# Optimization experiments

Hardware: AMD Instinct MI355X
Metric: run time of the kernel (lower is better)

The kernel has to match this reference:

```python
import jax, jax.numpy as jnp
import numpy as np

N = 50000       # nodes
E = 800000      # edges (avg degree 16)
R = 8           # relations
IN = 128        # in_channels
H = 128         # hidden_size
B = 10          # graphs in batch
NPG = N // B    # nodes per graph (equal-size graphs)
NEG_SLOPE = 0.2 # RGATConv default negative_slope


def setup_inputs() -> dict:
    key = jax.random.key(0)
    ks = jax.random.split(key, 12)
    s = 0.1
    x = jax.random.normal(ks[0], (N, IN), dtype=jnp.float32)
    edge_index = jax.random.randint(ks[1], (2, E), 0, N, dtype=jnp.int32)
    edge_type = jax.random.randint(ks[2], (E,), 0, R, dtype=jnp.int32)
    batch = jnp.repeat(jnp.arange(B, dtype=jnp.int32), NPG)
    W1 = jax.random.normal(ks[3], (R, IN, H), dtype=jnp.float32) * s
    q1 = jax.random.normal(ks[4], (H, 1), dtype=jnp.float32) * s
    k1 = jax.random.normal(ks[5], (H, 1), dtype=jnp.float32) * s
    b1 = jnp.zeros((H,), dtype=jnp.float32)
    W2 = jax.random.normal(ks[6], (R, H, H), dtype=jnp.float32) * s
    q2 = jax.random.normal(ks[7], (H, 1), dtype=jnp.float32) * s
    k2 = jax.random.normal(ks[8], (H, 1), dtype=jnp.float32) * s
    b2 = jnp.zeros((H,), dtype=jnp.float32)
    Wl = jax.random.normal(ks[9], (H, H), dtype=jnp.float32) * s
    bl = jnp.zeros((H,), dtype=jnp.float32)
    return dict(x=x, edge_index=edge_index, edge_type=edge_type, batch=batch,
                W1=W1, q1=q1, k1=k1, b1=b1, W2=W2, q2=q2, k2=k2, b2=b2,
                Wl=Wl, bl=bl)


def _rgat_conv(x, src, tgt, etype, W, q, k, b):
    # Per-relation transform once per node ([R,N,H]), then gather per edge;
    # mathematically identical to PyG's per-edge bmm but avoids the [E,in,H] blowup.
    xW = jnp.einsum('ni,rio->rno', x, W)          # [R, N, H]
    outi = xW[etype, tgt]                          # [E, H] transformed target feats
    outj = xW[etype, src]                          # [E, H] transformed source feats
    # additive self-attention, heads=1, dim=1
    alpha = jax.nn.leaky_relu(outi @ q + outj @ k, NEG_SLOPE)  # [E, 1]
    # across-relation segment softmax over incoming edges of each target node
    m = jax.ops.segment_max(alpha, tgt, num_segments=N)        # [N, 1]
    a = jnp.exp(alpha - m[tgt])
    den = jax.ops.segment_sum(a, tgt, num_segments=N)          # [N, 1]
    a = a / (den[tgt] + 1e-16)
    out = jax.ops.segment_sum(a * outj, tgt, num_segments=N)   # [N, H]
    return out + b


def reference(x, edge_index, edge_type, batch, W1, q1, k1, b1,
              W2, q2, k2, b2, Wl, bl):
    src, tgt = edge_index[0], edge_index[1]
    h = jax.nn.relu(_rgat_conv(x, src, tgt, edge_type, W1, q1, k1, b1))
    # dropout p=0 -> identity
    h = jax.nn.relu(_rgat_conv(h, src, tgt, edge_type, W2, q2, k2, b2))
    h = h @ Wl.T + bl                               # nn.Linear
    # to_dense_batch: batch is sorted with equal-size graphs of NPG nodes
    return h.reshape(B, NPG, H)
```

## Files before the change

### kernel.cpp

```cpp
#include <hip/hip_runtime.h>


typedef unsigned int uint;
typedef unsigned short ushort_t;

using bf16x8 = __attribute__((ext_vector_type(8))) __bf16;
using f32x4  = __attribute__((ext_vector_type(4))) float;

__device__ __forceinline__ ushort_t fToBf(float f) {
  uint u = __float_as_uint(f);
  u += 0x7FFFu + ((u >> 16) & 1);
  return (ushort_t)(u >> 16);
}
__device__ __forceinline__ float bfToF(ushort_t h) {
  return __uint_as_float(((uint)h) << 16);
}
__device__ __forceinline__ uint packBf(float a, float b) {
  return (uint)fToBf(a) | ((uint)fToBf(b) << 16);
}


__global__ void k_count(const int* __restrict__ tgt, int* __restrict__ deg, int E) {
  int e = blockIdx.x * 256 + threadIdx.x;
  if (e < E) atomicAdd(&deg[tgt[e]], 1);
}

__global__ void k_scanA(const int* __restrict__ deg, int* __restrict__ incl,
                        int* __restrict__ bsum, int n) {
  __shared__ int s[256];
  int tid = threadIdx.x;
  int i = blockIdx.x * 256 + tid;
  int v = (i < n) ? deg[i] : 0;
  s[tid] = v;
  __syncthreads();
  for (int off = 1; off < 256; off <<= 1) {
    int t = (tid >= off) ? s[tid - off] : 0;
    __syncthreads();
    s[tid] += t;
    __syncthreads();
  }
  if (i < n) incl[i] = s[tid];
  if (tid == 255) bsum[blockIdx.x] = s[255];
}

__global__ void k_scanB(int* __restrict__ bsum, int nb) {
  __shared__ int s[256];
  int tid = threadIdx.x;
  int v = (tid < nb) ? bsum[tid] : 0;
  s[tid] = v;
  __syncthreads();
  for (int off = 1; off < 256; off <<= 1) {
    int t = (tid >= off) ? s[tid - off] : 0;
    __syncthreads();
    s[tid] += t;
    __syncthreads();
  }
  if (tid < nb) bsum[tid] = s[tid] - v;
}

__global__ void k_scanC(const int* __restrict__ deg, const int* __restrict__ incl,
                        const int* __restrict__ bsum, int* __restrict__ rowptr,
                        int n, int E) {
  int i = blockIdx.x * 256 + threadIdx.x;
  if (i < n) {
    rowptr[i] = bsum[blockIdx.x] + incl[i] - deg[i];
    if (i == n - 1) rowptr[n] = E;
  }
}

__global__ void k_scatter(const int* __restrict__ src, const int* __restrict__ tgt,
                          const int* __restrict__ et, const int* __restrict__ rowptr,
                          int* __restrict__ cursor, int* __restrict__ sorted, int E) {
  int e = blockIdx.x * 256 + threadIdx.x;
  if (e >= E) return;
  int t = tgt[e];
  int pos = atomicAdd(&cursor[t], 1);
  sorted[rowptr[t] + pos] = src[e] | (et[e] << 16);
}


__global__ void k_wTf(const float* __restrict__ W1, const float* __restrict__ W2,
                      ushort_t* __restrict__ WTf) {
  int b = blockIdx.x * 4 + (threadIdx.x >> 6);
  int lane = threadIdx.x & 63;
  int layer = b >> 8;
  int r = (b >> 5) & 7;
  int f = b & 31;
  int mt = f >> 2, kb = f & 3;
  const float* W = layer ? W2 : W1;
  int col = mt * 16 + (lane & 15);
  int krow = kb * 32 + (lane >> 4) * 8;
  ushort_t* dst = WTf + ((size_t)b * 64 + lane) * 8;
  #pragma unroll
  for (int j = 0; j < 8; j++)
    dst[j] = fToBf(W[((size_t)r * 128 + krow + j) * 128 + col]);
}

__global__ void k_wqwk(const float* __restrict__ W1, const float* __restrict__ q1,
                       const float* __restrict__ k1, const float* __restrict__ W2,
                       const float* __restrict__ q2, const float* __restrict__ k2,
                       ushort_t* __restrict__ wqk) {
  int g = blockIdx.x * 256 + threadIdx.x;
  if (g >= 4096) return;
  int layer = g >> 11;
  int which = (g >> 10) & 1;
  int idx = g & 1023;
  const float* w = (layer ? W2 : W1) + (size_t)idx * 128;
  const float* v = layer ? (which ? k2 : q2) : (which ? k1 : q1);
  float s = 0.f;
  #pragma unroll 8
  for (int h = 0; h < 128; h++) s += w[h] * v[h];
  int r = idx >> 7, kin = idx & 127;
  wqk[(size_t)layer * 2048 + ((which << 3) + r) * 128 + kin] = fToBf(s);
}


template <bool F32IN>
__global__ __launch_bounds__(256, 4) void
k_xw(const void* __restrict__ Ain,
     const ushort_t* __restrict__ WTf,
     const ushort_t* __restrict__ Wqk,
     ushort_t* __restrict__ xW,
     float* __restrict__ stbl,
     int M) {
  __shared__ __align__(16) ushort_t wbuf[16384];
  int tid = threadIdx.x, wv = tid >> 6, lane = tid & 63;
  int l15 = lane & 15, quad = lane >> 4;
  int r = blockIdx.y;
  int node0 = blockIdx.x * 128 + wv * 32;

  {
    const ushort_t* src = WTf + (size_t)r * 16384;
    #pragma unroll
    for (int i = 0; i < 8; i++)
      *(int4*)(wbuf + (size_t)(tid + i * 256) * 8) =
          *(const int4*)(src + (size_t)(tid + i * 256) * 8);
  }

  bf16x8 bx[2][4];
  #pragma unroll
  for (int tile = 0; tile < 2; tile++) {
    int node = node0 + tile * 16 + l15;
    int nc = node < M ? node : M - 1;
    if (F32IN) {
      const float* row = (const float*)Ain + (size_t)nc * 128;
      #pragma unroll
      for (int kb = 0; kb < 4; kb++) {
        float4 a = *(const float4*)(row + kb * 32 + quad * 8);
        float4 b = *(const float4*)(row + kb * 32 + quad * 8 + 4);
        union { bf16x8 v; ushort_t u[8]; } t;
        t.u[0] = fToBf(a.x); t.u[1] = fToBf(a.y); t.u[2] = fToBf(a.z); t.u[3] = fToBf(a.w);
        t.u[4] = fToBf(b.x); t.u[5] = fToBf(b.y); t.u[6] = fToBf(b.z); t.u[7] = fToBf(b.w);
        bx[tile][kb] = t.v;
      }
    } else {
      const ushort_t* row = (const ushort_t*)Ain + (size_t)nc * 128;
      #pragma unroll
      for (int kb = 0; kb < 4; kb++)
        bx[tile][kb] = *(const bf16x8*)(row + kb * 32 + quad * 8);
    }
  }

  __syncthreads();

  uint2 po[2][8];
  #pragma unroll
  for (int mt = 0; mt < 8; mt++) {
    f32x4 a0 = {}, a1 = {};
    #pragma unroll
    for (int kb = 0; kb < 4; kb++) {
      bf16x8 af = *(const bf16x8*)(wbuf + (size_t)((mt * 4 + kb) * 64 + lane) * 8);
      a0 = __builtin_amdgcn_mfma_f32_16x16x32_bf16(af, bx[0][kb], a0, 0, 0, 0);
      a1 = __builtin_amdgcn_mfma_f32_16x16x32_bf16(af, bx[1][kb], a1, 0, 0, 0);
    }
    po[0][mt].x = packBf(a0[0], a0[1]); po[0][mt].y = packBf(a0[2], a0[3]);
    po[1][mt].x = packBf(a1[0], a1[1]); po[1][mt].y = packBf(a1[2], a1[3]);
  }
  #pragma unroll
  for (int tile = 0; tile < 2; tile++) {
    int node = node0 + tile * 16 + l15;
    if (node < M) {
      ushort_t* rowp = xW + ((size_t)r * M + node) * 128 + quad * 32;
      #pragma unroll
      for (int i = 0; i < 4; i++) {
        int4 v = {(int)po[tile][2 * i].x, (int)po[tile][2 * i].y,
                  (int)po[tile][2 * i + 1].x, (int)po[tile][2 * i + 1].y};
        *(int4*)(rowp + i * 8) = v;
      }
    }
  }

  if (r == 0) {
    bf16x8 aq[4];
    #pragma unroll
    for (int kb = 0; kb < 4; kb++)
      aq[kb] = *(const bf16x8*)(Wqk + (size_t)l15 * 128 + kb * 32 + quad * 8);
    #pragma unroll
    for (int tile = 0; tile < 2; tile++) {
      f32x4 s = {};
      #pragma unroll
      for (int kb = 0; kb < 4; kb++)
        s = __builtin_amdgcn_mfma_f32_16x16x32_bf16(aq[kb], bx[tile][kb], s, 0, 0, 0);
      int node = node0 + tile * 16 + l15;
      if (node < M) {
        float4 v = {s[0], s[1], s[2], s[3]};
        *(float4*)(stbl + (size_t)node * 16 + quad * 4) = v;
      }
    }
  }
}


#define ACC8(W_, V_)                                                     \
  acc[0] += W_ * bfToF((ushort_t)(V_.x & 0xFFFF));                       \
  acc[1] += W_ * bfToF((ushort_t)(V_.x >> 16));                          \
  acc[2] += W_ * bfToF((ushort_t)(V_.y & 0xFFFF));                       \
  acc[3] += W_ * bfToF((ushort_t)(V_.y >> 16));                          \
  acc[4] += W_ * bfToF((ushort_t)(V_.z & 0xFFFF));                       \
  acc[5] += W_ * bfToF((ushort_t)(V_.z >> 16));                          \
  acc[6] += W_ * bfToF((ushort_t)(V_.w & 0xFFFF));                       \
  acc[7] += W_ * bfToF((ushort_t)(V_.w >> 16));

__global__ __launch_bounds__(256) void
k_aggr(const ushort_t* __restrict__ feat,
       const float* __restrict__ stbl,
       const int* __restrict__ rowptr, const int* __restrict__ sorted,
       const float* __restrict__ bias, ushort_t* __restrict__ outp, int n) {
  int tid = threadIdx.x, wv = tid >> 6, lane = tid & 63;
  int t = blockIdx.x * 4 + wv;
  if (t >= n) return;
  int e0 = rowptr[t], e1 = rowptr[t + 1];
  int g4 = lane >> 4, fcol = lane & 15;

  float m = -INFINITY, den = 0.f;
  float acc[8] = {};

  for (int base = e0; base < e1; base += 64) {
    int cnt = min(64, e1 - base);
    float alpha = -INFINITY;
    int pk = 0;
    if (lane < cnt) {
      pk = sorted[base + lane];
      int s = pk & 0xFFFF, r = pk >> 16;
      float a = stbl[(size_t)t * 16 + r] + stbl[(size_t)s * 16 + 8 + r];
      alpha = (a >= 0.f) ? a : 0.2f * a;
    }
    float cm = alpha;
    #pragma unroll
    for (int off = 32; off; off >>= 1) cm = fmaxf(cm, __shfl_xor(cm, off, 64));
    float nm = fmaxf(m, cm);
    float sc = __expf(m - nm);
    den *= sc;
    #pragma unroll
    for (int i = 0; i < 8; i++) acc[i] *= sc;
    float w = (lane < cnt) ? __expf(alpha - nm) : 0.f;
    float ws = w;
    #pragma unroll
    for (int off = 32; off; off >>= 1) ws += __shfl_xor(ws, off, 64);
    den += ws;
    m = nm;

    for (int g = 0; g < cnt; g += 16) {
      int i0 = g + g4;
      float w0 = __shfl(w, i0, 64);
      float w1 = __shfl(w, i0 + 4, 64);
      float w2 = __shfl(w, i0 + 8, 64);
      float w3 = __shfl(w, i0 + 12, 64);
      int p0 = __shfl(pk, i0, 64);
      int p1 = __shfl(pk, i0 + 4, 64);
      int p2 = __shfl(pk, i0 + 8, 64);
      int p3 = __shfl(pk, i0 + 12, 64);
      const uint4* r0 = (const uint4*)(feat + (size_t)((p0 >> 16) * n + (p0 & 0xFFFF)) * 128) + fcol;
      const uint4* r1 = (const uint4*)(feat + (size_t)((p1 >> 16) * n + (p1 & 0xFFFF)) * 128) + fcol;
      const uint4* r2 = (const uint4*)(feat + (size_t)((p2 >> 16) * n + (p2 & 0xFFFF)) * 128) + fcol;
      const uint4* r3 = (const uint4*)(feat + (size_t)((p3 >> 16) * n + (p3 & 0xFFFF)) * 128) + fcol;
      uint4 v0 = *r0;
      uint4 v1 = *r1;
      uint4 v2 = *r2;
      uint4 v3 = *r3;
      ACC8(w0, v0)
      ACC8(w1, v1)
      ACC8(w2, v2)
      ACC8(w3, v3)
    }
  }

  #pragma unroll
  for (int i = 0; i < 8; i++) acc[i] += __shfl_xor(acc[i], 16, 64);
  #pragma unroll
  for (int i = 0; i < 8; i++) acc[i] += __shfl_xor(acc[i], 32, 64);

  float inv = (den > 0.f) ? 1.f / (den + 1e-16f) : 0.f;
  int base0 = (fcol & 3) * 32 + (fcol >> 2) * 4;
  float4 ba = *(const float4*)(bias + base0);
  float4 bb = *(const float4*)(bias + base0 + 16);
  uint2 oa, ob;
  oa.x = packBf(fmaxf(acc[0] * inv + ba.x, 0.f), fmaxf(acc[1] * inv + ba.y, 0.f));
  oa.y = packBf(fmaxf(acc[2] * inv + ba.z, 0.f), fmaxf(acc[3] * inv + ba.w, 0.f));
  ob.x = packBf(fmaxf(acc[4] * inv + bb.x, 0.f), fmaxf(acc[5] * inv + bb.y, 0.f));
  ob.y = packBf(fmaxf(acc[6] * inv + bb.z, 0.f), fmaxf(acc[7] * inv + bb.w, 0.f));
  if (lane < 16) {
    *(uint2*)(outp + (size_t)t * 128 + base0) = oa;
    *(uint2*)(outp + (size_t)t * 128 + base0 + 16) = ob;
  }
}


#define LDA 136

__global__ __launch_bounds__(256) void
k_gemmL(const ushort_t* __restrict__ A, const float* __restrict__ Wl,
        float* __restrict__ Cout, const float* __restrict__ bias, int M) {
  __shared__ ushort_t As[64 * LDA];
  __shared__ ushort_t Bs[128 * LDA];
  int tid = threadIdx.x;
  int row0 = blockIdx.x * 64;
  for (int c = tid; c < 1024; c += 256) {
    int r = c >> 4, off = (c & 15) * 8;
    int4 v = {0, 0, 0, 0};
    if (row0 + r < M) v = *(const int4*)(A + (size_t)(row0 + r) * 128 + off);
    *(int4*)(As + r * LDA + off) = v;
  }
  for (int c = tid; c < 2048; c += 256) {
    int nn = c >> 4, off = (c & 15) * 8;
    float4 a = *(const float4*)(Wl + (size_t)nn * 128 + off);
    float4 b = *(const float4*)(Wl + (size_t)nn * 128 + off + 4);
    ushort_t* d = Bs + nn * LDA + off;
    d[0] = fToBf(a.x); d[1] = fToBf(a.y); d[2] = fToBf(a.z); d[3] = fToBf(a.w);
    d[4] = fToBf(b.x); d[5] = fToBf(b.y); d[6] = fToBf(b.z); d[7] = fToBf(b.w);
  }
  __syncthreads();
  int wv = tid >> 6, lane = tid & 63;
  int l15 = lane & 15, quad = lane >> 4;
  int wr = wv * 16;
  bf16x8 afr[4];
  #pragma unroll
  for (int kb = 0; kb < 4; kb++)
    afr[kb] = *reinterpret_cast<const bf16x8*>(As + (wr + l15) * LDA + kb * 32 + quad * 8);
  f32x4 acc[8] = {};
  #pragma unroll
  for (int ct = 0; ct < 8; ct++)
    #pragma unroll
    for (int kb = 0; kb < 4; kb++) {
      bf16x8 bfr = *reinterpret_cast<const bf16x8*>(Bs + (ct * 16 + l15) * LDA + kb * 32 + quad * 8);
      acc[ct] = __builtin_amdgcn_mfma_f32_16x16x32_bf16(afr[kb], bfr, acc[ct], 0, 0, 0);
    }
  #pragma unroll
  for (int ct = 0; ct < 8; ct++)
    #pragma unroll
    for (int reg = 0; reg < 4; reg++) {
      int rr = row0 + wr + quad * 4 + reg;
      if (rr < M) Cout[(size_t)rr * 128 + ct * 16 + l15] = acc[ct][reg] + bias[ct * 16 + l15];
    }
}


extern "C" void kernel_launch(void* const* d_in, const int* in_sizes, int n_in,
                              void* d_out, int out_size, void* d_ws, size_t ws_size,
                              hipStream_t stream) {
  const float* x   = (const float*)d_in[0];
  const int* ei    = (const int*)d_in[1];
  const int* etype = (const int*)d_in[2];
  const float* W1  = (const float*)d_in[4];
  const float* q1  = (const float*)d_in[5];
  const float* k1  = (const float*)d_in[6];
  const float* b1  = (const float*)d_in[7];
  const float* W2  = (const float*)d_in[8];
  const float* q2  = (const float*)d_in[9];
  const float* k2  = (const float*)d_in[10];
  const float* b2  = (const float*)d_in[11];
  const float* Wl  = (const float*)d_in[12];
  const float* bl  = (const float*)d_in[13];
  float* out       = (float*)d_out;

  const int N = in_sizes[0] / 128;
  const int E = in_sizes[2];

  char* ws = (char*)d_ws;
  size_t off = 0;
  auto alloc = [&](size_t bytes) {
    size_t o = off;
    off = (off + bytes + 255) & ~(size_t)255;
    return o;
  };

  ushort_t* xW    = (ushort_t*)(ws + alloc((size_t)8 * N * 128 * 2));
  ushort_t* h1    = (ushort_t*)(ws + alloc((size_t)N * 128 * 2));
  ushort_t* h2    = (ushort_t*)(ws + alloc((size_t)N * 128 * 2));
  ushort_t* WTf   = (ushort_t*)(ws + alloc((size_t)2 * 8 * 16384 * 2));
  ushort_t* wqk   = (ushort_t*)(ws + alloc(2 * 16 * 128 * 2));
  float* stblA    = (float*)(ws + alloc((size_t)N * 16 * 4));
  float* stblB    = (float*)(ws + alloc((size_t)N * 16 * 4));
  int* deg        = (int*)(ws + alloc((size_t)N * 4));
  int* cursor     = (int*)(ws + alloc((size_t)N * 4));
  int* incl       = (int*)(ws + alloc((size_t)N * 4));
  int* rowptr     = (int*)(ws + alloc((size_t)(N + 1) * 4));
  int* bsum       = (int*)(ws + alloc(256 * 4));
  int* sorted     = (int*)(ws + alloc((size_t)E * 4));
  (void)ws_size; (void)n_in; (void)out_size;

  const int* srcp = ei;
  const int* tgtp = ei + E;

  int gE = (E + 255) / 256;
  int gN = (N + 255) / 256;
  int gW = (N + 3) / 4;
  int NB = (N + 127) / 128;
  int gL = (N + 63) / 64;

  hipMemsetAsync(deg, 0, (size_t)N * 4, stream);
  hipMemsetAsync(cursor, 0, (size_t)N * 4, stream);
  k_count<<<gE, 256, 0, stream>>>(tgtp, deg, E);
  k_scanA<<<gN, 256, 0, stream>>>(deg, incl, bsum, N);
  k_scanB<<<1, 256, 0, stream>>>(bsum, gN);
  k_scanC<<<gN, 256, 0, stream>>>(deg, incl, bsum, rowptr, N, E);
  k_scatter<<<gE, 256, 0, stream>>>(srcp, tgtp, etype, rowptr, cursor, sorted, E);

  k_wTf<<<128, 256, 0, stream>>>(W1, W2, WTf);
  k_wqwk<<<16, 256, 0, stream>>>(W1, q1, k1, W2, q2, k2, wqk);

  k_xw<true><<<dim3(NB, 8), 256, 0, stream>>>(x, WTf, wqk, xW, stblA, N);
  k_aggr<<<gW, 256, 0, stream>>>(xW, stblA, rowptr, sorted, b1, h1, N);

  k_xw<false><<<dim3(NB, 8), 256, 0, stream>>>(h1, WTf + (size_t)8 * 16384,
                                               wqk + 2048, xW, stblB, N);
  k_aggr<<<gW, 256, 0, stream>>>(xW, stblB, rowptr, sorted, b2, h2, N);

  k_gemmL<<<gL, 256, 0, stream>>>(h2, Wl, out, bl, N);
}
```

Before: 412.0 us.

## Aggregate raw features per relation before transforming, replacing per-relation xW materialization

Instead of computing xW for all 8 relations (an 8xNx128 bf16 tensor) and gathering transformed rows per edge, edges are now sorted by (target, relation). The kernel gathers raw input features weighted by attention into a per-node, per-relation buffer, then applies the relation weights with a single MFMA GEMM over the concatenated K=1024 dimension. Attention scores are still computed from the precomputed W·q / W·k projections. This cuts the per-edge gather from 8 relation-specific tables to one shared table and removes the large xW write. In exchange it adds an N×1024 intermediate buffer, a serial per-edge loop with one lane per feature pair, and a larger CSR sort over N*8 bins.

```diff
diff --git a/kernel.cpp b/kernel.cpp
--- a/kernel.cpp
+++ b/kernel.cpp
@@ -20,9 +20,10 @@
 }
 
 
-__global__ void k_count(const int* __restrict__ tgt, int* __restrict__ deg, int E) {
+__global__ void k_count2(const int* __restrict__ tgt, const int* __restrict__ et,
+                         int* __restrict__ deg2, int E) {
   int e = blockIdx.x * 256 + threadIdx.x;
-  if (e < E) atomicAdd(&deg[tgt[e]], 1);
+  if (e < E) atomicAdd(&deg2[tgt[e] * 8 + et[e]], 1);
 }
 
 __global__ void k_scanA(const int* __restrict__ deg, int* __restrict__ incl,
@@ -43,19 +44,29 @@
   if (tid == 255) bsum[blockIdx.x] = s[255];
 }
 
-__global__ void k_scanB(int* __restrict__ bsum, int nb) {
+__global__ void k_scanB2(int* __restrict__ bsum, int nb) {
   __shared__ int s[256];
+  __shared__ int carry;
   int tid = threadIdx.x;
-  int v = (tid < nb) ? bsum[tid] : 0;
-  s[tid] = v;
+  if (tid == 0) carry = 0;
   __syncthreads();
-  for (int off = 1; off < 256; off <<= 1) {
-    int t = (tid >= off) ? s[tid - off] : 0;
-    __syncthreads();
-    s[tid] += t;
-    __syncthreads();
-  }
-  if (tid < nb) bsum[tid] = s[tid] - v;
+  for (int base = 0; base < nb; base += 256) {
+    int i = base + tid;
+    int v = (i < nb) ? bsum[i] : 0;
+    s[tid] = v;
+    __syncthreads();
+    for (int off = 1; off < 256; off <<= 1) {
+      int t = (tid >= off) ? s[tid - off] : 0;
+      __syncthreads();
+      s[tid] += t;
+      __syncthreads();
+    }
+    int c = carry;
+    if (i < nb) bsum[i] = c + s[tid] - v;
+    __syncthreads();
+    if (tid == 255) carry = c + s[255];
+    __syncthreads();
+  }
 }
 
 __global__ void k_scanC(const int* __restrict__ deg, const int* __restrict__ incl,
@@ -68,32 +79,27 @@
   }
 }
 
-__global__ void k_scatter(const int* __restrict__ src, const int* __restrict__ tgt,
-                          const int* __restrict__ et, const int* __restrict__ rowptr,
-                          int* __restrict__ cursor, int* __restrict__ sorted, int E) {
+__global__ void k_scatter2(const int* __restrict__ src, const int* __restrict__ tgt,
+                           const int* __restrict__ et, const int* __restrict__ rowptr2,
+                           int* __restrict__ cursor2, int* __restrict__ sorted, int E) {
   int e = blockIdx.x * 256 + threadIdx.x;
   if (e >= E) return;
-  int t = tgt[e];
-  int pos = atomicAdd(&cursor[t], 1);
-  sorted[rowptr[t] + pos] = src[e] | (et[e] << 16);
-}
-
-
-__global__ void k_wTf(const float* __restrict__ W1, const float* __restrict__ W2,
-                      ushort_t* __restrict__ WTf) {
-  int b = blockIdx.x * 4 + (threadIdx.x >> 6);
-  int lane = threadIdx.x & 63;
-  int layer = b >> 8;
-  int r = (b >> 5) & 7;
-  int f = b & 31;
-  int mt = f >> 2, kb = f & 3;
-  const float* W = layer ? W2 : W1;
-  int col = mt * 16 + (lane & 15);
-  int krow = kb * 32 + (lane >> 4) * 8;
-  ushort_t* dst = WTf + ((size_t)b * 64 + lane) * 8;
-  #pragma unroll
-  for (int j = 0; j < 8; j++)
-    dst[j] = fToBf(W[((size_t)r * 128 + krow + j) * 128 + col]);
+  int t8r = tgt[e] * 8 + et[e];
+  int pos = atomicAdd(&cursor2[t8r], 1);
+  sorted[rowptr2[t8r] + pos] = src[e] | (et[e] << 16);
+}
+
+
+__global__ void k_wsT(const float* __restrict__ W1, const float* __restrict__ W2,
+                      ushort_t* __restrict__ WsT) {
+  int idx = blockIdx.x * 256 + threadIdx.x;
+  int n = idx & 127;
+  int k = (idx >> 7) & 127;
+  int rl = idx >> 14;
+  const float* W = (rl >> 3) ? W2 : W1;
+  int r = rl & 7;
+  float v = W[((size_t)r * 128 + k) * 128 + n];
+  WsT[((size_t)rl * 128 + n) * 128 + k] = fToBf(v);
 }
 
 __global__ void k_wqwk(const float* __restrict__ W1, const float* __restrict__ q1,
@@ -116,26 +122,15 @@
 
 
 template <bool F32IN>
-__global__ __launch_bounds__(256, 4) void
-k_xw(const void* __restrict__ Ain,
-     const ushort_t* __restrict__ WTf,
-     const ushort_t* __restrict__ Wqk,
-     ushort_t* __restrict__ xW,
-     float* __restrict__ stbl,
-     int M) {
-  __shared__ __align__(16) ushort_t wbuf[16384];
+__global__ __launch_bounds__(256) void
+k_score(const void* __restrict__ Ain,
+        const ushort_t* __restrict__ Wqk,
+        ushort_t* __restrict__ xb,
+        float* __restrict__ stbl,
+        int M) {
   int tid = threadIdx.x, wv = tid >> 6, lane = tid & 63;
   int l15 = lane & 15, quad = lane >> 4;
-  int r = blockIdx.y;
   int node0 = blockIdx.x * 128 + wv * 32;
-
-  {
-    const ushort_t* src = WTf + (size_t)r * 16384;
-    #pragma unroll
-    for (int i = 0; i < 8; i++)
-      *(int4*)(wbuf + (size_t)(tid + i * 256) * 8) =
-          *(const int4*)(src + (size_t)(tid + i * 256) * 8);
-  }
 
   bf16x8 bx[2][4];
   #pragma unroll
@@ -161,152 +156,183 @@
     }
   }
 
-  __syncthreads();
-
-  uint2 po[2][8];
-  #pragma unroll
-  for (int mt = 0; mt < 8; mt++) {
-    f32x4 a0 = {}, a1 = {};
-    #pragma unroll
-    for (int kb = 0; kb < 4; kb++) {
-      bf16x8 af = *(const bf16x8*)(wbuf + (size_t)((mt * 4 + kb) * 64 + lane) * 8);
-      a0 = __builtin_amdgcn_mfma_f32_16x16x32_bf16(af, bx[0][kb], a0, 0, 0, 0);
-      a1 = __builtin_amdgcn_mfma_f32_16x16x32_bf16(af, bx[1][kb], a1, 0, 0, 0);
-    }
-    po[0][mt].x = packBf(a0[0], a0[1]); po[0][mt].y = packBf(a0[2], a0[3]);
-    po[1][mt].x = packBf(a1[0], a1[1]); po[1][mt].y = packBf(a1[2], a1[3]);
-  }
+  if (F32IN) {
+    #pragma unroll
+    for (int tile = 0; tile < 2; tile++) {
+      int node = node0 + tile * 16 + l15;
+      if (node < M) {
+        #pragma unroll
+        for (int kb = 0; kb < 4; kb++)
+          *(bf16x8*)(xb + (size_t)node * 128 + kb * 32 + quad * 8) = bx[tile][kb];
+      }
+    }
+  }
+
+  bf16x8 aq[4];
+  #pragma unroll
+  for (int kb = 0; kb < 4; kb++)
+    aq[kb] = *(const bf16x8*)(Wqk + (size_t)l15 * 128 + kb * 32 + quad * 8);
   #pragma unroll
   for (int tile = 0; tile < 2; tile++) {
+    f32x4 s = {};
+    #pragma unroll
+    for (int kb = 0; kb < 4; kb++)
+      s = __builtin_amdgcn_mfma_f32_16x16x32_bf16(aq[kb], bx[tile][kb], s, 0, 0, 0);
     int node = node0 + tile * 16 + l15;
     if (node < M) {
-      ushort_t* rowp = xW + ((size_t)r * M + node) * 128 + quad * 32;
-      #pragma unroll
-      for (int i = 0; i < 4; i++) {
-        int4 v = {(int)po[tile][2 * i].x, (int)po[tile][2 * i].y,
-                  (int)po[tile][2 * i + 1].x, (int)po[tile][2 * i + 1].y};
-        *(int4*)(rowp + i * 8) = v;
-      }
-    }
-  }
-
-  if (r == 0) {
-    bf16x8 aq[4];
-    #pragma unroll
-    for (int kb = 0; kb < 4; kb++)
-      aq[kb] = *(const bf16x8*)(Wqk + (size_t)l15 * 128 + kb * 32 + quad * 8);
-    #pragma unroll
-    for (int tile = 0; tile < 2; tile++) {
-      f32x4 s = {};
-      #pragma unroll
-      for (int kb = 0; kb < 4; kb++)
-        s = __builtin_amdgcn_mfma_f32_16x16x32_bf16(aq[kb], bx[tile][kb], s, 0, 0, 0);
-      int node = node0 + tile * 16 + l15;
-      if (node < M) {
-        float4 v = {s[0], s[1], s[2], s[3]};
-        *(float4*)(stbl + (size_t)node * 16 + quad * 4) = v;
-      }
-    }
-  }
-}
-
-
-#define ACC8(W_, V_)                                                     \
-  acc[0] += W_ * bfToF((ushort_t)(V_.x & 0xFFFF));                       \
-  acc[1] += W_ * bfToF((ushort_t)(V_.x >> 16));                          \
-  acc[2] += W_ * bfToF((ushort_t)(V_.y & 0xFFFF));                       \
-  acc[3] += W_ * bfToF((ushort_t)(V_.y >> 16));                          \
-  acc[4] += W_ * bfToF((ushort_t)(V_.z & 0xFFFF));                       \
-  acc[5] += W_ * bfToF((ushort_t)(V_.z >> 16));                          \
-  acc[6] += W_ * bfToF((ushort_t)(V_.w & 0xFFFF));                       \
-  acc[7] += W_ * bfToF((ushort_t)(V_.w >> 16));
+      float4 v = {s[0], s[1], s[2], s[3]};
+      *(float4*)(stbl + (size_t)node * 16 + quad * 4) = v;
+    }
+  }
+}
+
 
 __global__ __launch_bounds__(256) void
-k_aggr(const ushort_t* __restrict__ feat,
-       const float* __restrict__ stbl,
-       const int* __restrict__ rowptr, const int* __restrict__ sorted,
-       const float* __restrict__ bias, ushort_t* __restrict__ outp, int n) {
+k_gather(const ushort_t* __restrict__ feat,
+         const float* __restrict__ stbl,
+         const int* __restrict__ rp2,
+         const int* __restrict__ sorted,
+         ushort_t* __restrict__ g,
+         int n) {
+  __shared__ int   s_pk[4][64];
+  __shared__ float s_al[4][64];
+  __shared__ float s_w[4][64];
   int tid = threadIdx.x, wv = tid >> 6, lane = tid & 63;
   int t = blockIdx.x * 4 + wv;
   if (t >= n) return;
-  int e0 = rowptr[t], e1 = rowptr[t + 1];
-  int g4 = lane >> 4, fcol = lane & 15;
+  int e0 = rp2[t * 8], e1 = rp2[t * 8 + 8];
 
   float m = -INFINITY, den = 0.f;
-  float acc[8] = {};
-
   for (int base = e0; base < e1; base += 64) {
     int cnt = min(64, e1 - base);
     float alpha = -INFINITY;
-    int pk = 0;
     if (lane < cnt) {
-      pk = sorted[base + lane];
+      int pk = sorted[base + lane];
       int s = pk & 0xFFFF, r = pk >> 16;
       float a = stbl[(size_t)t * 16 + r] + stbl[(size_t)s * 16 + 8 + r];
       alpha = (a >= 0.f) ? a : 0.2f * a;
+      s_pk[wv][lane] = pk;
+      s_al[wv][lane] = alpha;
     }
     float cm = alpha;
     #pragma unroll
     for (int off = 32; off; off >>= 1) cm = fmaxf(cm, __shfl_xor(cm, off, 64));
     float nm = fmaxf(m, cm);
-    float sc = __expf(m - nm);
-    den *= sc;
-    #pragma unroll
-    for (int i = 0; i < 8; i++) acc[i] *= sc;
     float w = (lane < cnt) ? __expf(alpha - nm) : 0.f;
     float ws = w;
     #pragma unroll
     for (int off = 32; off; off >>= 1) ws += __shfl_xor(ws, off, 64);
-    den += ws;
+    den = den * __expf(m - nm) + ws;
     m = nm;
-
-    for (int g = 0; g < cnt; g += 16) {
-      int i0 = g + g4;
-      float w0 = __shfl(w, i0, 64);
-      float w1 = __shfl(w, i0 + 4, 64);
-      float w2 = __shfl(w, i0 + 8, 64);
-      float w3 = __shfl(w, i0 + 12, 64);
-      int p0 = __shfl(pk, i0, 64);
-      int p1 = __shfl(pk, i0 + 4, 64);
-      int p2 = __shfl(pk, i0 + 8, 64);
-      int p3 = __shfl(pk, i0 + 12, 64);
-      const uint4* r0 = (const uint4*)(feat + (size_t)((p0 >> 16) * n + (p0 & 0xFFFF)) * 128) + fcol;
-      const uint4* r1 = (const uint4*)(feat + (size_t)((p1 >> 16) * n + (p1 & 0xFFFF)) * 128) + fcol;
-      const uint4* r2 = (const uint4*)(feat + (size_t)((p2 >> 16) * n + (p2 & 0xFFFF)) * 128) + fcol;
-      const uint4* r3 = (const uint4*)(feat + (size_t)((p3 >> 16) * n + (p3 & 0xFFFF)) * 128) + fcol;
-      uint4 v0 = *r0;
-      uint4 v1 = *r1;
-      uint4 v2 = *r2;
-      uint4 v3 = *r3;
-      ACC8(w0, v0)
-      ACC8(w1, v1)
-      ACC8(w2, v2)
-      ACC8(w3, v3)
-    }
-  }
-
-  #pragma unroll
-  for (int i = 0; i < 8; i++) acc[i] += __shfl_xor(acc[i], 16, 64);
-  #pragma unroll
-  for (int i = 0; i < 8; i++) acc[i] += __shfl_xor(acc[i], 32, 64);
-
+  }
   float inv = (den > 0.f) ? 1.f / (den + 1e-16f) : 0.f;
-  int base0 = (fcol & 3) * 32 + (fcol >> 2) * 4;
-  float4 ba = *(const float4*)(bias + base0);
-  float4 bb = *(const float4*)(bias + base0 + 16);
-  uint2 oa, ob;
-  oa.x = packBf(fmaxf(acc[0] * inv + ba.x, 0.f), fmaxf(acc[1] * inv + ba.y, 0.f));
-  oa.y = packBf(fmaxf(acc[2] * inv + ba.z, 0.f), fmaxf(acc[3] * inv + ba.w, 0.f));
-  ob.x = packBf(fmaxf(acc[4] * inv + bb.x, 0.f), fmaxf(acc[5] * inv + bb.y, 0.f));
-  ob.y = packBf(fmaxf(acc[6] * inv + bb.z, 0.f), fmaxf(acc[7] * inv + bb.w, 0.f));
-  if (lane < 16) {
-    *(uint2*)(outp + (size_t)t * 128 + base0) = oa;
-    *(uint2*)(outp + (size_t)t * 128 + base0 + 16) = ob;
-  }
+
+  const uint* fx = (const uint*)feat;
+  uint* grow = (uint*)(g + (size_t)t * 1024);
+  float ga = 0.f, gb = 0.f;
+  int rw = 0;
+  bool stored = (e1 - e0) <= 64;
+
+  for (int base = e0; base < e1; base += 64) {
+    int cnt = min(64, e1 - base);
+    if (lane < cnt) {
+      int pk; float a;
+      if (stored) {
+        pk = s_pk[wv][lane];
+        a = s_al[wv][lane];
+      } else {
+        pk = sorted[base + lane];
+        int s = pk & 0xFFFF, r = pk >> 16;
+        a = stbl[(size_t)t * 16 + r] + stbl[(size_t)s * 16 + 8 + r];
+        a = (a >= 0.f) ? a : 0.2f * a;
+        s_pk[wv][lane] = pk;
+      }
+      s_w[wv][lane] = __expf(a - m) * inv;
+    }
+    for (int i = 0; i < cnt; i++) {
+      int pk = s_pk[wv][i];
+      float w = s_w[wv][i];
+      int r = pk >> 16;
+      if (r != rw) {
+        grow[rw * 64 + lane] = packBf(ga, gb);
+        for (int z = rw + 1; z < r; z++) grow[z * 64 + lane] = 0u;
+        rw = r; ga = 0.f; gb = 0.f;
+      }
+      uint v = fx[(size_t)(pk & 0xFFFF) * 64 + lane];
+      ga = __builtin_fmaf(w, bfToF((ushort_t)(v & 0xFFFF)), ga);
+      gb = __builtin_fmaf(w, bfToF((ushort_t)(v >> 16)), gb);
+    }
+  }
+  grow[rw * 64 + lane] = packBf(ga, gb);
+  for (int z = rw + 1; z < 8; z++) grow[z * 64 + lane] = 0u;
 }
 
 
 #define LDA 136
+
+__global__ __launch_bounds__(256) void
+k_out(const ushort_t* __restrict__ g,
+      const ushort_t* __restrict__ WsT,
+      const float* __restrict__ bias,
+      ushort_t* __restrict__ h,
+      int M) {
+  __shared__ ushort_t As[64 * LDA];
+  __shared__ ushort_t Bs[128 * LDA];
+  int tid = threadIdx.x, wv = tid >> 6, lane = tid & 63;
+  int l15 = lane & 15, quad = lane >> 4;
+  int row0 = blockIdx.x * 64;
+  int wr = wv * 16;
+  f32x4 acc[8] = {};
+
+  for (int r = 0; r < 8; r++) {
+    {
+      int row = tid >> 2, seg = tid & 3;
+      int4 z = {0, 0, 0, 0};
+      int4 v0 = z, v1 = z, v2 = z, v3 = z;
+      if (row0 + row < M) {
+        const int4* src = (const int4*)(g + ((size_t)(row0 + row) * 8 + r) * 128 + seg * 32);
+        v0 = src[0]; v1 = src[1]; v2 = src[2]; v3 = src[3];
+      }
+      int4* dst = (int4*)(As + row * LDA + seg * 32);
+      dst[0] = v0; dst[1] = v1; dst[2] = v2; dst[3] = v3;
+    }
+    {
+      const int4* src = (const int4*)(WsT + (size_t)r * 16384);
+      for (int u = tid; u < 512; u += 256) {
+        int rowb = u >> 2, seg = u & 3;
+        int4* dst = (int4*)(Bs + rowb * LDA + seg * 32);
+        #pragma unroll
+        for (int j = 0; j < 4; j++) dst[j] = src[rowb * 16 + seg * 4 + j];
+      }
+    }
+    __syncthreads();
+
+    bf16x8 afr[4];
+    #pragma unroll
+    for (int kb = 0; kb < 4; kb++)
+      afr[kb] = *(const bf16x8*)(As + (wr + l15) * LDA + kb * 32 + quad * 8);
+    #pragma unroll
+    for (int ct = 0; ct < 8; ct++)
+      #pragma unroll
+      for (int kb = 0; kb < 4; kb++) {
+        bf16x8 bfr = *(const bf16x8*)(Bs + (ct * 16 + l15) * LDA + kb * 32 + quad * 8);
+        acc[ct] = __builtin_amdgcn_mfma_f32_16x16x32_bf16(afr[kb], bfr, acc[ct], 0, 0, 0);
+      }
+    __syncthreads();
+  }
+
+  #pragma unroll
+  for (int ct = 0; ct < 8; ct++) {
+    float b = bias[ct * 16 + l15];
+    #pragma unroll
+    for (int reg = 0; reg < 4; reg++) {
+      int rr = row0 + wr + quad * 4 + reg;
+      if (rr < M)
+        h[(size_t)rr * 128 + ct * 16 + l15] = fToBf(fmaxf(acc[ct][reg] + b, 0.f));
+    }
+  }
+}
+
 
 __global__ __launch_bounds__(256) void
 k_gemmL(const ushort_t* __restrict__ A, const float* __restrict__ Wl,
@@ -384,47 +410,48 @@
     return o;
   };
 
-  ushort_t* xW    = (ushort_t*)(ws + alloc((size_t)8 * N * 128 * 2));
+  ushort_t* g     = (ushort_t*)(ws + alloc((size_t)N * 1024 * 2));
   ushort_t* h1    = (ushort_t*)(ws + alloc((size_t)N * 128 * 2));
-  ushort_t* h2    = (ushort_t*)(ws + alloc((size_t)N * 128 * 2));
-  ushort_t* WTf   = (ushort_t*)(ws + alloc((size_t)2 * 8 * 16384 * 2));
+  ushort_t* xbh2  = (ushort_t*)(ws + alloc((size_t)N * 128 * 2));
+  ushort_t* WsT   = (ushort_t*)(ws + alloc((size_t)2 * 8 * 16384 * 2));
   ushort_t* wqk   = (ushort_t*)(ws + alloc(2 * 16 * 128 * 2));
-  float* stblA    = (float*)(ws + alloc((size_t)N * 16 * 4));
-  float* stblB    = (float*)(ws + alloc((size_t)N * 16 * 4));
-  int* deg        = (int*)(ws + alloc((size_t)N * 4));
-  int* cursor     = (int*)(ws + alloc((size_t)N * 4));
-  int* incl       = (int*)(ws + alloc((size_t)N * 4));
-  int* rowptr     = (int*)(ws + alloc((size_t)(N + 1) * 4));
-  int* bsum       = (int*)(ws + alloc(256 * 4));
+  float* stbl     = (float*)(ws + alloc((size_t)N * 16 * 4));
+  int* deg2       = (int*)(ws + alloc((size_t)N * 8 * 4));
+  int* cursor2    = (int*)(ws + alloc((size_t)N * 8 * 4));
+  int* incl2      = (int*)(ws + alloc((size_t)N * 8 * 4));
+  int* rowptr2    = (int*)(ws + alloc((size_t)(N * 8 + 1) * 4));
+  int* bsum       = (int*)(ws + alloc(2048 * 4));
   int* sorted     = (int*)(ws + alloc((size_t)E * 4));
   (void)ws_size; (void)n_in; (void)out_size;
 
   const int* srcp = ei;
   const int* tgtp = ei + E;
 
-  int gE = (E + 255) / 256;
-  int gN = (N + 255) / 256;
-  int gW = (N + 3) / 4;
-  int NB = (N + 127) / 128;
-  int gL = (N + 63) / 64;
-
-  hipMemsetAsync(deg, 0, (size_t)N * 4, stream);
-  hipMemsetAsync(cursor, 0, (size_t)N * 4, stream);
-  k_count<<<gE, 256, 0, stream>>>(tgtp, deg, E);
-  k_scanA<<<gN, 256, 0, stream>>>(deg, incl, bsum, N);
-  k_scanB<<<1, 256, 0, stream>>>(bsum, gN);
-  k_scanC<<<gN, 256, 0, stream>>>(deg, incl, bsum, rowptr, N, E);
-  k_scatter<<<gE, 256, 0, stream>>>(srcp, tgtp, etype, rowptr, cursor, sorted, E);
-
-  k_wTf<<<128, 256, 0, stream>>>(W1, W2, WTf);
+  int n2 = N * 8;
+  int gE  = (E + 255) / 256;
+  int gN2 = (n2 + 255) / 256;
+  int gS  = (N + 127) / 128;
+  int gG  = (N + 3) / 4;
+  int gO  = (N + 63) / 64;
+
+  hipMemsetAsync(deg2, 0, (size_t)n2 * 4, stream);
+  hipMemsetAsync(cursor2, 0, (size_t)n2 * 4, stream);
+  k_count2<<<gE, 256, 0, stream>>>(tgtp, etype, deg2, E);
+  k_scanA<<<gN2, 256, 0, stream>>>(deg2, incl2, bsum, n2);
+  k_scanB2<<<1, 256, 0, stream>>>(bsum, gN2);
+  k_scanC<<<gN2, 256, 0, stream>>>(deg2, incl2, bsum, rowptr2, n2, E);
+  k_scatter2<<<gE, 256, 0, stream>>>(srcp, tgtp, etype, rowptr2, cursor2, sorted, E);
+
+  k_wsT<<<1024, 256, 0, stream>>>(W1, W2, WsT);
   k_wqwk<<<16, 256, 0, stream>>>(W1, q1, k1, W2, q2, k2, wqk);
 
-  k_xw<true><<<dim3(NB, 8), 256, 0, stream>>>(x, WTf, wqk, xW, stblA, N);
-  k_aggr<<<gW, 256, 0, stream>>>(xW, stblA, rowptr, sorted, b1, h1, N);
-
-  k_xw<false><<<dim3(NB, 8), 256, 0, stream>>>(h1, WTf + (size_t)8 * 16384,
-                                               wqk + 2048, xW, stblB, N);
-  k_aggr<<<gW, 256, 0, stream>>>(xW, stblB, rowptr, sorted, b2, h2, N);
-
-  k_gemmL<<<gL, 256, 0, stream>>>(h2, Wl, out, bl, N);
-}
+  k_score<true><<<gS, 256, 0, stream>>>(x, wqk, xbh2, stbl, N);
+  k_gather<<<gG, 256, 0, stream>>>(xbh2, stbl, rowptr2, sorted, g, N);
+  k_out<<<gO, 256, 0, stream>>>(g, WsT, b1, h1, N);
+
+  k_score<false><<<gS, 256, 0, stream>>>(h1, wqk + 2048, nullptr, stbl, N);
+  k_gather<<<gG, 256, 0, stream>>>(h1, stbl, rowptr2, sorted, g, N);
+  k_out<<<gO, 256, 0, stream>>>(g, WsT + (size_t)8 * 16384, b2, xbh2, N);
+
+  k_gemmL<<<gO, 256, 0, stream>>>(xbh2, Wl, out, bl, N);
+}
```

After: 476.2 us. +15.6%, slower.
